# Kernel optimization log

Measured on AMD Instinct MI355X. Metric: run time of the kernel, lower is better.

The kernel has to match this reference:

```python
import jax, jax.numpy as jnp
import numpy as np
from jax import lax

DIM = 192
HEADS = 4
B, H, W = 4, 128, 128


def _conv1x1(x, w):
    # x: (B,C,H,W), w: (O,C,1,1)
    return lax.conv_general_dilated(x, w, (1, 1), 'VALID',
                                    dimension_numbers=('NCHW', 'OIHW', 'NCHW'))


def _dwconv3(x, w):
    # depthwise 3x3, padding 1; w: (C,1,3,3)
    return lax.conv_general_dilated(x, w, (1, 1), ((1, 1), (1, 1)),
                                    feature_group_count=x.shape[1],
                                    dimension_numbers=('NCHW', 'OIHW', 'NCHW'))


def setup_inputs() -> dict:
    key = jax.random.key(0)
    ks = jax.random.split(key, 5)
    x = jax.random.normal(ks[0], (B, DIM, H, W), jnp.float32)
    w_qkv = jax.random.normal(ks[1], (3 * DIM, DIM, 1, 1), jnp.float32) * 0.02
    w_dw = jax.random.normal(ks[2], (3 * DIM, 1, 3, 3), jnp.float32) * 0.02
    w_out = jax.random.normal(ks[3], (DIM, DIM, 1, 1), jnp.float32) * 0.02
    temperature = jnp.ones((HEADS, 1, 1), jnp.float32)
    attn_w = jax.random.uniform(ks[4], (4,), jnp.float32)
    return {'x': x, 'w_qkv': w_qkv, 'w_dw': w_dw, 'w_out': w_out,
            'temperature': temperature, 'attn_w': attn_w}


def _topk_softmax(attn, k):
    # mask keeps the top-k entries per row (matches torch topk+scatter+where)
    idx = lax.top_k(attn, k)[1]                                   # (b,h,C,k)
    mask = jax.nn.one_hot(idx, attn.shape[-1], dtype=attn.dtype).sum(-2)  # (b,h,C,C)
    masked = jnp.where(mask > 0, attn, -jnp.inf)
    return jax.nn.softmax(masked, axis=-1)


def reference(x, w_qkv, w_dw, w_out, temperature, attn_w):
    b, c, h, w = x.shape
    qkv = _dwconv3(_conv1x1(x, w_qkv), w_dw)
    q, k, v = jnp.split(qkv, 3, axis=1)

    def to_heads(t):
        return t.reshape(b, HEADS, c // HEADS, h * w)  # (b,head,C,hw)

    q, k, v = to_heads(q), to_heads(k), to_heads(v)
    # F.normalize along the token (last) dim, eps=1e-12
    q = q / jnp.maximum(jnp.linalg.norm(q, axis=-1, keepdims=True), 1e-12)
    k = k / jnp.maximum(jnp.linalg.norm(k, axis=-1, keepdims=True), 1e-12)

    C = q.shape[2]
    attn = jnp.einsum('bhcn,bhdn->bhcd', q, k) * temperature  # (b,h,C,C)

    out = None
    for i, kk in enumerate([C // 2, C * 2 // 3, C * 3 // 4, C * 4 // 5]):
        a = _topk_softmax(attn, kk)
        o = jnp.einsum('bhcd,bhdn->bhcn', a, v) * attn_w[i]
        out = o if out is None else out + o

    out = out.reshape(b, c, h, w)
    return _conv1x1(out, w_out)
```

## Files before the change

### kernel.cpp

```cpp
#include <hip/hip_runtime.h>
#include <hip/hip_bf16.h>

#define HW   16384
#define WIDTH 128
#define CIN  192
#define C3   576
#define NB   4
#define CH   48

typedef __attribute__((ext_vector_type(8))) __bf16 bf16x8;
typedef __attribute__((ext_vector_type(4))) float f32x4;

__device__ __forceinline__ unsigned short f2bf(float f) {
  unsigned u = __float_as_uint(f);
  unsigned r = (u + 0x7fffu + ((u >> 16) & 1u)) >> 16;
  return (unsigned short)r;
}
__device__ __forceinline__ float bf2f(unsigned short h) {
  return __uint_as_float((unsigned)h << 16);
}

__global__ void k_wpack(const float* __restrict__ w, unsigned short* __restrict__ wp)
{
  const int bid = blockIdx.x;
  const int mt = bid / 6, kg = bid - 6 * mt;
  const int l = threadIdx.x;
  const int m = mt * 16 + (l & 15);
  const int g = l >> 4;
  unsigned short vh[8], vl[8];
#pragma unroll
  for (int j = 0; j < 8; j++) {
    int k = kg * 32 + (g << 2) + (j & 3) + ((j >> 2) << 4);
    float x = w[m * 192 + k];
    vh[j] = f2bf(x);
    vl[j] = f2bf(x - bf2f(vh[j]));
  }
  *(uint4*)(wp + ((size_t)bid * 64 + l) * 8) = *(uint4*)vh;
  *(uint4*)(wp + 110592 + ((size_t)bid * 64 + l) * 8) = *(uint4*)vl;
}

__global__ __launch_bounds__(512) void k_gemm_sb(
    const float* __restrict__ Bsrc, const unsigned short* __restrict__ Afrag,
    float* __restrict__ out, size_t bBatch, size_t aBatch, size_t outBatch,
    size_t aLoOff)
{
  __shared__ unsigned short Bt[2][8][16][100];
  const int b = blockIdx.z, mb = blockIdx.y;
  const int pBase = blockIdx.x * 128;
  const int t = threadIdx.x;
  const int lane = t & 63, w = t >> 6;
  const int wm = w >> 1, wn = w & 1;
  const int g = lane >> 4, c = lane & 15;
  const float* Bp = Bsrc + (size_t)b * bBatch + pBase;
  const unsigned short* Ap = Afrag + (size_t)b * aBatch;
  const int mtBase = mb * 12 + wm * 3;

  f32x4 acc[3][4];
#pragma unroll
  for (int i = 0; i < 3; i++)
#pragma unroll
    for (int nf = 0; nf < 4; nf++) acc[i][nf] = f32x4{0.f, 0.f, 0.f, 0.f};

  for (int kh = 0; kh < 2; kh++) {
    if (kh) __syncthreads();
    {
      const int kr = lane >> 2, nc = (lane & 3) * 4;
      const float* src = Bp + w * 16 + nc;
#pragma unroll
      for (int i = 0; i < 6; i++) {
        int kl = i * 16 + kr;
        float4 v = *(const float4*)&src[(size_t)(kh * 96 + kl) * HW];
        float xs[4] = {v.x, v.y, v.z, v.w};
#pragma unroll
        for (int q = 0; q < 4; q++) {
          unsigned short hh = f2bf(xs[q]);
          Bt[0][w][nc + q][kl] = hh;
          Bt[1][w][nc + q][kl] = f2bf(xs[q] - bf2f(hh));
        }
      }
    }
    __syncthreads();
#pragma unroll
    for (int ks = 0; ks < 3; ks++) {
      const int kg = kh * 3 + ks;
      bf16x8 afh[3], afl[3];
#pragma unroll
      for (int i = 0; i < 3; i++) {
        size_t fo = (((size_t)(mtBase + i) * 6 + kg) * 64 + lane) * 8;
        afh[i] = __builtin_bit_cast(bf16x8, *(const uint4*)(Ap + fo));
        afl[i] = __builtin_bit_cast(bf16x8, *(const uint4*)(Ap + aLoOff + fo));
      }
      const int k0 = ks * 32 + g * 4;
#pragma unroll
      for (int nf = 0; nf < 4; nf++) {
        const int ns = wn * 4 + nf;
        const unsigned short* ch = &Bt[0][ns][c][0];
        const unsigned short* cl = &Bt[1][ns][c][0];
        uint2 h0 = *(const uint2*)(ch + k0);
        uint2 h1 = *(const uint2*)(ch + k0 + 16);
        uint2 l0 = *(const uint2*)(cl + k0);
        uint2 l1 = *(const uint2*)(cl + k0 + 16);
        uint4 bw;
        bw.x = h0.x; bw.y = h0.y; bw.z = h1.x; bw.w = h1.y;
        bf16x8 bfh = __builtin_bit_cast(bf16x8, bw);
        bw.x = l0.x; bw.y = l0.y; bw.z = l1.x; bw.w = l1.y;
        bf16x8 bfl = __builtin_bit_cast(bf16x8, bw);
#pragma unroll
        for (int i = 0; i < 3; i++) {
          acc[i][nf] = __builtin_amdgcn_mfma_f32_16x16x32_bf16(afh[i], bfl, acc[i][nf], 0, 0, 0);
          acc[i][nf] = __builtin_amdgcn_mfma_f32_16x16x32_bf16(afl[i], bfh, acc[i][nf], 0, 0, 0);
          acc[i][nf] = __builtin_amdgcn_mfma_f32_16x16x32_bf16(afh[i], bfh, acc[i][nf], 0, 0, 0);
        }
      }
    }
  }

  const int r0 = g * 4, c0 = c;
  float* op = out + (size_t)b * outBatch + pBase + wn * 64 + c0;
#pragma unroll
  for (int i = 0; i < 3; i++) {
    int mrow = (mtBase + i) * 16 + r0;
#pragma unroll
    for (int nf = 0; nf < 4; nf++)
#pragma unroll
      for (int r = 0; r < 4; r++)
        op[(size_t)(mrow + r) * HW + nf * 16] = acc[i][nf][r];
  }
}

__global__ __launch_bounds__(256) void k_dwconv_norm(
    float* __restrict__ buf, const float* __restrict__ wdw, float* __restrict__ inorm)
{
  const int bo = blockIdx.x;
  const int ch = bo % C3;
  const int b  = bo / C3;
  float* plane = buf + (size_t)bo * HW;
  float wv[9];
#pragma unroll
  for (int i = 0; i < 9; i++) wv[i] = wdw[ch * 9 + i];

  __shared__ float ring[16][128];
  __shared__ float red[4];
  const int tx = threadIdx.x & 31;
  const int ty = threadIdx.x >> 5;
  const int x0 = tx * 4;

  *(float4*)&ring[ty][x0] = *(const float4*)&plane[ty * WIDTH + x0];
  if (ty == 0) *(float4*)&ring[8][x0] = *(const float4*)&plane[8 * WIDTH + x0];

  float ssum = 0.f;

  for (int c = 0; c < 16; c++) {
    __syncthreads();
    const int y = c * 8 + ty;
    float a0 = 0.f, a1 = 0.f, a2 = 0.f, a3 = 0.f;
#pragma unroll
    for (int dy = 0; dy < 3; dy++) {
      int yy = y + dy - 1;
      if (yy < 0 || yy > 127) continue;
      const float* r = ring[yy & 15];
      float4 cc = *(const float4*)&r[x0];
      float left  = (x0 > 0) ? r[x0 - 1] : 0.f;
      float right = (x0 + 4 < WIDTH) ? r[x0 + 4] : 0.f;
      float w0 = wv[dy * 3 + 0], w1 = wv[dy * 3 + 1], w2 = wv[dy * 3 + 2];
      a0 += w0 * left + w1 * cc.x + w2 * cc.y;
      a1 += w0 * cc.x + w1 * cc.y + w2 * cc.z;
      a2 += w0 * cc.y + w1 * cc.z + w2 * cc.w;
      a3 += w0 * cc.z + w1 * cc.w + w2 * right;
    }
    __syncthreads();
    *(float4*)&plane[y * WIDTH + x0] = make_float4(a0, a1, a2, a3);
    ssum += a0 * a0 + a1 * a1 + a2 * a2 + a3 * a3;
    if (c < 15) {
      int rrow = c * 8 + 9 + ty;
      if (rrow < 128)
        *(float4*)&ring[rrow & 15][x0] = *(const float4*)&plane[rrow * WIDTH + x0];
    }
  }

  if (ch < 384) {
    for (int off = 32; off; off >>= 1) ssum += __shfl_down(ssum, off, 64);
    if ((threadIdx.x & 63) == 0) red[threadIdx.x >> 6] = ssum;
    __syncthreads();
    if (threadIdx.x == 0) {
      float tot = red[0] + red[1] + red[2] + red[3];
      inorm[b * 384 + ch] = 1.0f / fmaxf(sqrtf(tot), 1e-12f);
    }
  }
}

__global__ __launch_bounds__(256) void k_attn_part(
    const float* __restrict__ qkv, float* __restrict__ part)
{
  const int bh = blockIdx.y;
  const int b = bh >> 2, h = bh & 3;
  const int pbase = blockIdx.x * 1024;
  const float* qb = qkv + ((size_t)b * C3 +       h * CH) * HW + pbase;
  const float* kb = qkv + ((size_t)b * C3 + 192 + h * CH) * HW + pbase;
  __shared__ float Ql[48][33], Kl[48][33];
  const int t = threadIdx.x;
  const int c0 = (t & 15) * 3, d0 = (t >> 4) * 3;
  float acc[3][3];
#pragma unroll
  for (int i = 0; i < 3; i++)
#pragma unroll
    for (int j = 0; j < 3; j++) acc[i][j] = 0.f;

  for (int chk = 0; chk < 32; chk++) {
    const int pp0 = chk * 32;
#pragma unroll
    for (int i = 0; i < 6; i++) {
      int lin = t + i * 256;
      int cc = lin >> 5, pp = lin & 31;
      Ql[cc][pp] = qb[(size_t)cc * HW + pp0 + pp];
      Kl[cc][pp] = kb[(size_t)cc * HW + pp0 + pp];
    }
    __syncthreads();
#pragma unroll
    for (int pp = 0; pp < 32; pp++) {
      float q0 = Ql[c0][pp], q1 = Ql[c0 + 1][pp], q2 = Ql[c0 + 2][pp];
      float k0v = Kl[d0][pp], k1v = Kl[d0 + 1][pp], k2v = Kl[d0 + 2][pp];
      acc[0][0] += q0 * k0v; acc[0][1] += q0 * k1v; acc[0][2] += q0 * k2v;
      acc[1][0] += q1 * k0v; acc[1][1] += q1 * k1v; acc[1][2] += q1 * k2v;
      acc[2][0] += q2 * k0v; acc[2][1] += q2 * k1v; acc[2][2] += q2 * k2v;
    }
    __syncthreads();
  }
  float* pb = part + ((size_t)blockIdx.x * 16 + bh) * 2304;
#pragma unroll
  for (int i = 0; i < 3; i++)
#pragma unroll
    for (int j = 0; j < 3; j++)
      pb[(c0 + i) * 48 + d0 + j] = acc[i][j];
}

__global__ __launch_bounds__(64) void k_topk_combine(
    const float* __restrict__ part, const float* __restrict__ inorm,
    const float* __restrict__ temp, const float* __restrict__ attnw,
    float* __restrict__ A)
{
  const int bh = blockIdx.x;
  const int b = bh >> 2, h = bh & 3;
  __shared__ float Sv[48][49];
  const float tmp = temp[h];
  for (int lin = threadIdx.x; lin < 2304; lin += 64) {
    float s = 0.f;
    for (int ps = 0; ps < 16; ps++)
      s += part[((size_t)ps * 16 + bh) * 2304 + lin];
    int c = lin / 48, d = lin - (lin / 48) * 48;
    Sv[c][d] = s * inorm[b * 384 + h * 48 + c]
                 * inorm[b * 384 + 192 + h * 48 + d] * tmp;
  }
  __syncthreads();
  if (threadIdx.x < 48) {
    const int c = threadIdx.x;
    float m = -3.4e38f;
    for (int d = 0; d < 48; d++) m = fmaxf(m, Sv[c][d]);
    unsigned long long mk0 = 0, mk1 = 0, mk2 = 0, mk3 = 0;
    float S0 = 0.f, S1 = 0.f, S2 = 0.f, S3 = 0.f;
    for (int d = 0; d < 48; d++) {
      float vd = Sv[c][d];
      int cnt = 0;
      for (int d2 = 0; d2 < 48; d2++) {
        float v2 = Sv[c][d2];
        cnt += (v2 > vd) || (v2 == vd && d2 < d);
      }
      float e = expf(vd - m);
      if (cnt < 24) { mk0 |= 1ull << d; S0 += e; }
      if (cnt < 32) { mk1 |= 1ull << d; S1 += e; }
      if (cnt < 36) { mk2 |= 1ull << d; S2 += e; }
      if (cnt < 38) { mk3 |= 1ull << d; S3 += e; }
    }
    float w0 = attnw[0] / S0, w1 = attnw[1] / S1;
    float w2 = attnw[2] / S2, w3 = attnw[3] / S3;
    float* Ao = A + ((size_t)bh * 48 + c) * 48;
    for (int d = 0; d < 48; d++) {
      float e = expf(Sv[c][d] - m);
      float a = 0.f;
      if ((mk0 >> d) & 1) a += w0 * e;
      if ((mk1 >> d) & 1) a += w1 * e;
      if ((mk2 >> d) & 1) a += w2 * e;
      if ((mk3 >> d) & 1) a += w3 * e;
      Ao[d] = a;
    }
  }
}

__global__ __launch_bounds__(256) void k_mbuild2(
    const float* __restrict__ wout, const float* __restrict__ A,
    unsigned short* __restrict__ mp)
{
  const int mt = blockIdx.x, b = blockIdx.y;
  __shared__ float Ml[16][193];
  const int t = threadIdx.x;
  const int o = t >> 4, jg = t & 15;
#pragma unroll
  for (int e = 0; e < 12; e++) {
    int j = jg * 12 + e;
    int h = j / 48, d = j - h * 48;
    const float* wrow = wout + (mt * 16 + o) * 192 + h * 48;
    const float* Ab = A + ((size_t)(b * 4 + h) * 48) * 48 + d;
    float s = 0.f;
#pragma unroll
    for (int c2 = 0; c2 < 48; c2++) s += wrow[c2] * Ab[c2 * 48];
    Ml[o][j] = s;
  }
  __syncthreads();
  unsigned short* mpo = mp + ((size_t)b * 12 + mt) * 3072;
#pragma unroll
  for (int e = 0; e < 12; e++) {
    int idx = t * 12 + e;
    int kg = idx >> 9, rem = idx & 511, l = rem >> 3, j = rem & 7;
    int k = kg * 32 + ((l >> 4) << 2) + (j & 3) + ((j >> 2) << 4);
    float x = Ml[l & 15][k];
    unsigned short h = f2bf(x);
    mpo[idx] = h;
    mpo[147456 + idx] = f2bf(x - bf2f(h));
  }
}

extern "C" void kernel_launch(void* const* d_in, const int* in_sizes, int n_in,
                              void* d_out, int out_size, void* d_ws, size_t ws_size,
                              hipStream_t stream)
{
  const float* x     = (const float*)d_in[0];
  const float* wqkv  = (const float*)d_in[1];
  const float* wdw   = (const float*)d_in[2];
  const float* wout  = (const float*)d_in[3];
  const float* temp  = (const float*)d_in[4];
  const float* attnw = (const float*)d_in[5];
  float* outp = (float*)d_out;
  float* ws = (float*)d_ws;

  float* qkvbuf    = ws;
  float* inorm     = ws + 37748736;
  float* attn_part = ws + 37750272;
  float* Acomb     = ws + 38340096;
  unsigned short* wp16 = (unsigned short*)(ws + 38376960);
  unsigned short* mp16 = (unsigned short*)(ws + 38487552);

  k_wpack<<<216, 64, 0, stream>>>(wqkv, wp16);

  k_gemm_sb<<<dim3(128, 3, NB), 512, 0, stream>>>(
      x, wp16, qkvbuf, (size_t)CIN * HW, 0, (size_t)C3 * HW, (size_t)110592);

  k_dwconv_norm<<<NB * C3, 256, 0, stream>>>(qkvbuf, wdw, inorm);

  k_attn_part<<<dim3(16, 16), 256, 0, stream>>>(qkvbuf, attn_part);

  k_topk_combine<<<16, 64, 0, stream>>>(attn_part, inorm, temp, attnw, Acomb);

  k_mbuild2<<<dim3(12, NB), 256, 0, stream>>>(wout, Acomb, mp16);

  k_gemm_sb<<<dim3(128, 1, NB), 512, 0, stream>>>(
      qkvbuf + (size_t)384 * HW, mp16, outp,
      (size_t)C3 * HW, (size_t)36864, (size_t)CIN * HW, (size_t)147456);
}
```

Baseline: 457.9 us.

## Split partial-sum reduction into its own kernel and parallelize top-k per element

The 16-way partial attention sum moves into a separate 144-block kernel instead of running inside a 16-block, 64-thread kernel. The top-k/softmax kernel now uses 256 threads: each wavefront handles 12 rows with one lane per column, and the row max and four masked softmax sums are done with wave shuffles. This targets a tiny serial kernel where 48 threads each did 48x48 rank comparisons. It costs one extra launch and a global round trip for the reduced attention matrix.

```diff
diff --git a/kernel.cpp b/kernel.cpp
--- a/kernel.cpp
+++ b/kernel.cpp
@@ -234,8 +234,18 @@
       pb[(c0 + i) * 48 + d0 + j] = acc[i][j];
 }
 
-__global__ __launch_bounds__(64) void k_topk_combine(
-    const float* __restrict__ part, const float* __restrict__ inorm,
+__global__ __launch_bounds__(256) void k_attn_reduce(
+    const float* __restrict__ part, float* __restrict__ attn)
+{
+  int idx = blockIdx.x * 256 + threadIdx.x;
+  float s = 0.f;
+#pragma unroll
+  for (int ps = 0; ps < 16; ps++) s += part[(size_t)ps * 36864 + idx];
+  attn[idx] = s;
+}
+
+__global__ __launch_bounds__(256) void k_topk2(
+    const float* __restrict__ attn, const float* __restrict__ inorm,
     const float* __restrict__ temp, const float* __restrict__ attnw,
     float* __restrict__ A)
 {
@@ -243,45 +253,48 @@
   const int b = bh >> 2, h = bh & 3;
   __shared__ float Sv[48][49];
   const float tmp = temp[h];
-  for (int lin = threadIdx.x; lin < 2304; lin += 64) {
-    float s = 0.f;
-    for (int ps = 0; ps < 16; ps++)
-      s += part[((size_t)ps * 16 + bh) * 2304 + lin];
-    int c = lin / 48, d = lin - (lin / 48) * 48;
-    Sv[c][d] = s * inorm[b * 384 + h * 48 + c]
-                 * inorm[b * 384 + 192 + h * 48 + d] * tmp;
+  const int tid = threadIdx.x;
+  const float* ar = attn + (size_t)bh * 2304;
+#pragma unroll
+  for (int k = 0; k < 9; k++) {
+    int i = tid + k * 256;
+    int c = i / 48, d = i - (i / 48) * 48;
+    Sv[c][d] = ar[i] * inorm[b * 384 + h * 48 + c]
+                     * inorm[b * 384 + 192 + h * 48 + d] * tmp;
   }
   __syncthreads();
-  if (threadIdx.x < 48) {
-    const int c = threadIdx.x;
-    float m = -3.4e38f;
-    for (int d = 0; d < 48; d++) m = fmaxf(m, Sv[c][d]);
-    unsigned long long mk0 = 0, mk1 = 0, mk2 = 0, mk3 = 0;
-    float S0 = 0.f, S1 = 0.f, S2 = 0.f, S3 = 0.f;
-    for (int d = 0; d < 48; d++) {
-      float vd = Sv[c][d];
-      int cnt = 0;
-      for (int d2 = 0; d2 < 48; d2++) {
-        float v2 = Sv[c][d2];
-        cnt += (v2 > vd) || (v2 == vd && d2 < d);
-      }
-      float e = expf(vd - m);
-      if (cnt < 24) { mk0 |= 1ull << d; S0 += e; }
-      if (cnt < 32) { mk1 |= 1ull << d; S1 += e; }
-      if (cnt < 36) { mk2 |= 1ull << d; S2 += e; }
-      if (cnt < 38) { mk3 |= 1ull << d; S3 += e; }
-    }
-    float w0 = attnw[0] / S0, w1 = attnw[1] / S1;
-    float w2 = attnw[2] / S2, w3 = attnw[3] / S3;
-    float* Ao = A + ((size_t)bh * 48 + c) * 48;
-    for (int d = 0; d < 48; d++) {
-      float e = expf(Sv[c][d] - m);
+  const float w0 = attnw[0], w1 = attnw[1], w2 = attnw[2], w3 = attnw[3];
+  const int wv = tid >> 6, d = tid & 63;
+  for (int r = 0; r < 12; r++) {
+    const int c = wv * 12 + r;
+    float vd = (d < 48) ? Sv[c][d] : -3.4e38f;
+    float m = vd;
+#pragma unroll
+    for (int off = 32; off; off >>= 1) m = fmaxf(m, __shfl_xor(m, off, 64));
+    int cnt = 0;
+    for (int d2 = 0; d2 < 48; d2++) {
+      float v2 = Sv[c][d2];
+      cnt += (v2 > vd) || (v2 == vd && d2 < d);
+    }
+    float e = (d < 48) ? expf(vd - m) : 0.f;
+    float S0 = (cnt < 24) ? e : 0.f;
+    float S1 = (cnt < 32) ? e : 0.f;
+    float S2 = (cnt < 36) ? e : 0.f;
+    float S3 = (cnt < 38) ? e : 0.f;
+#pragma unroll
+    for (int off = 32; off; off >>= 1) {
+      S0 += __shfl_xor(S0, off, 64);
+      S1 += __shfl_xor(S1, off, 64);
+      S2 += __shfl_xor(S2, off, 64);
+      S3 += __shfl_xor(S3, off, 64);
+    }
+    if (d < 48) {
       float a = 0.f;
-      if ((mk0 >> d) & 1) a += w0 * e;
-      if ((mk1 >> d) & 1) a += w1 * e;
-      if ((mk2 >> d) & 1) a += w2 * e;
-      if ((mk3 >> d) & 1) a += w3 * e;
-      Ao[d] = a;
+      if (cnt < 24) a += w0 / S0 * e;
+      if (cnt < 32) a += w1 / S1 * e;
+      if (cnt < 36) a += w2 / S2 * e;
+      if (cnt < 38) a += w3 / S3 * e;
+      A[((size_t)bh * 48 + c) * 48 + d] = a;
     }
   }
 }
@@ -338,6 +351,7 @@
   float* Acomb     = ws + 38340096;
   unsigned short* wp16 = (unsigned short*)(ws + 38376960);
   unsigned short* mp16 = (unsigned short*)(ws + 38487552);
+  float* attn_raw  = ws + 38635008;
 
   k_wpack<<<216, 64, 0, stream>>>(wqkv, wp16);
 
@@ -348,7 +362,9 @@
 
   k_attn_part<<<dim3(16, 16), 256, 0, stream>>>(qkvbuf, attn_part);
 
-  k_topk_combine<<<16, 64, 0, stream>>>(attn_part, inorm, temp, attnw, Acomb);
+  k_attn_reduce<<<144, 256, 0, stream>>>(attn_part, attn_raw);
+
+  k_topk2<<<16, 256, 0, stream>>>(attn_raw, inorm, temp, attnw, Acomb);
 
   k_mbuild2<<<dim3(12, NB), 256, 0, stream>>>(wout, Acomb, mp16);
 
```

New measurement: 368.3 us. 19.6% less time.
